# Kernel tuning notes

Measured on AMD Instinct MI355X. Metric: run time of the kernel, lower is better.

Reference implementation:

```python
import jax, jax.numpy as jnp
import numpy as np

D_MODEL = 1024
N_HEADS = 16
HEAD_DIM = D_MODEL // N_HEADS
B, L, E = 2, 2048, 256


def _linear_params(key, d_out, d_in):
    kw, kb = jax.random.split(key)
    lim = 1.0 / np.sqrt(d_in)
    W = jax.random.uniform(kw, (d_out, d_in), jnp.float32, -lim, lim)
    b = jax.random.uniform(kb, (d_out,), jnp.float32, -lim, lim)
    return W, b


def setup_inputs() -> dict:
    key = jax.random.key(0)
    ks = jax.random.split(key, 10)
    x = jax.random.normal(ks[0], (B, L, D_MODEL), jnp.float32)
    kg_embeds = jax.random.normal(ks[1], (B, E, D_MODEL), jnp.float32)
    Wq, bq = _linear_params(ks[2], D_MODEL, D_MODEL)
    Wk, bk = _linear_params(ks[3], D_MODEL, D_MODEL)
    Wv, bv = _linear_params(ks[4], D_MODEL, D_MODEL)
    Wo, bo = _linear_params(ks[5], D_MODEL, D_MODEL)
    Wkk, bkk = _linear_params(ks[6], D_MODEL, D_MODEL)
    Wkv, bkv = _linear_params(ks[7], D_MODEL, D_MODEL)
    Wg, bg = _linear_params(ks[8], D_MODEL, 2 * D_MODEL)
    return {"x": x, "kg_embeds": kg_embeds,
            "Wq": Wq, "bq": bq, "Wk": Wk, "bk": bk, "Wv": Wv, "bv": bv,
            "Wkk": Wkk, "bkk": bkk, "Wkv": Wkv, "bkv": bkv,
            "Wo": Wo, "bo": bo, "Wg": Wg, "bg": bg}


def _heads(t):
    # [B, S, D] -> [B, H, S, hd]
    Bb, S, _ = t.shape
    return t.reshape(Bb, S, N_HEADS, HEAD_DIM).transpose(0, 2, 1, 3)


def reference(x, kg_embeds, Wq, bq, Wk, bk, Wv, bv, Wkk, bkk, Wkv, bkv, Wo, bo, Wg, bg):
    scale = HEAD_DIM ** -0.5
    q = _heads(x @ Wq.T + bq)                      # [B,H,L,hd]
    k = _heads(x @ Wk.T + bk)
    v = _heads(x @ Wv.T + bv)
    k_kg = _heads(kg_embeds @ Wkk.T + bkk)         # [B,H,E,hd]
    v_kg = _heads(kg_embeds @ Wkv.T + bkv)
    k_aug = jnp.concatenate([k, k_kg], axis=2)     # [B,H,L+E,hd]
    v_aug = jnp.concatenate([v, v_kg], axis=2)
    scores = jnp.einsum('bhld,bhmd->bhlm', q, k_aug) * scale  # [B,H,L,L+E]
    attn = jax.nn.softmax(scores, axis=-1)
    out = jnp.einsum('bhlm,bhmd->bhld', attn, v_aug)           # [B,H,L,hd]
    out = out.transpose(0, 2, 1, 3).reshape(x.shape)            # [B,L,D]
    kg_global = jnp.broadcast_to(kg_embeds.mean(axis=1, keepdims=True), x.shape)
    gate = jax.nn.sigmoid(jnp.concatenate([out, kg_global], axis=-1) @ Wg.T + bg)
    return gate * (out @ Wo.T + bo) + (1.0 - gate) * x
```

## Files before the change

### kernel.cpp

```cpp
#include <hip/hip_runtime.h>
#include <stdint.h>

typedef unsigned short ushort_t;
typedef __attribute__((ext_vector_type(8))) short short8;
typedef __attribute__((ext_vector_type(4))) short short4v;
typedef __attribute__((ext_vector_type(4))) float f32x4;
typedef __attribute__((ext_vector_type(4))) unsigned uintx4;

#define DEV static __device__ __forceinline__

DEV unsigned short f2bf(float f) {
  unsigned u = __builtin_bit_cast(unsigned, f);
  u += 0x7fffu + ((u >> 16) & 1u);
  return (unsigned short)(u >> 16);
}
DEV float bf2f(unsigned short b) {
  return __builtin_bit_cast(float, (unsigned)b << 16);
}

DEV void gl16(const void* g, void* l) {
  __builtin_amdgcn_global_load_lds(
      (__attribute__((address_space(1))) char*)(unsigned long long)g,
      (__attribute__((address_space(3))) char*)(unsigned)(unsigned long long)l,
      16, 0, 0);
}

DEV f32x4 mfma_bf16(short8 a, short8 b, f32x4 c) {
  return __builtin_amdgcn_mfma_f32_16x16x32_bf16(a, b, c, 0, 0, 0);
}

DEV unsigned cvtpk(float lo, float hi) {
  unsigned r;
  asm("v_cvt_pk_bf16_f32 %0, %1, %2" : "=v"(r) : "v"(lo), "v"(hi));
  return r;
}
DEV void swap_net(unsigned& a, unsigned& b) {
  asm("v_permlane32_swap_b32 %0, %1" : "+v"(a), "+v"(b));
  asm("v_permlane16_swap_b32 %0, %1" : "+v"(a), "+v"(b));
}
DEV float redmax4(float x) {
  unsigned a = __builtin_bit_cast(unsigned, x), b = a;
  asm("v_permlane16_swap_b32 %0, %1" : "+v"(a), "+v"(b));
  float y = fmaxf(__builtin_bit_cast(float, a), __builtin_bit_cast(float, b));
  unsigned c = __builtin_bit_cast(unsigned, y), d = c;
  asm("v_permlane32_swap_b32 %0, %1" : "+v"(c), "+v"(d));
  return fmaxf(__builtin_bit_cast(float, c), __builtin_bit_cast(float, d));
}
DEV float lanebcast(float v, int srclane) {
  return __builtin_bit_cast(float,
      __builtin_amdgcn_ds_bpermute(srclane * 4, __builtin_bit_cast(int, v)));
}

__global__ __launch_bounds__(256) void k_cvt_all(
    const float* __restrict__ x, const float* __restrict__ kg,
    const float* __restrict__ Wq, const float* __restrict__ Wk, const float* __restrict__ Wv,
    const float* __restrict__ Wkk, const float* __restrict__ Wkv,
    const float* __restrict__ Wo, const float* __restrict__ Wg,
    ushort_t* __restrict__ xh, ushort_t* __restrict__ kgh,
    ushort_t* __restrict__ WB1, ushort_t* __restrict__ WB2, ushort_t* __restrict__ WB3) {
  const int b = blockIdx.x;
  if (b >= 10752) {
    const int i = (b - 10752) * 256 + threadIdx.x;
    const int r = i >> 8, c = (i & 255) * 4;
    const float4 v = *(const float4*)(Wg + (size_t)r * 2048 + c);
    short4v o;
    o.x = (short)f2bf(v.x); o.y = (short)f2bf(v.y); o.z = (short)f2bf(v.z); o.w = (short)f2bf(v.w);
    *(short4v*)(WB3 + 1048576 + (size_t)r * 1024 + c) = o;
    return;
  }
  const float* src;
  ushort_t* dst;
  int off;
  if (b < 4096)       { src = x;   dst = xh;            off = b; }
  else if (b < 4608)  { src = kg;  dst = kgh;           off = b - 4096; }
  else if (b < 5632)  { src = Wq;  dst = WB1;           off = b - 4608; }
  else if (b < 6656)  { src = Wk;  dst = WB1 + 1048576; off = b - 5632; }
  else if (b < 7680)  { src = Wv;  dst = WB1 + 2097152; off = b - 6656; }
  else if (b < 8704)  { src = Wkk; dst = WB2;           off = b - 7680; }
  else if (b < 9728)  { src = Wkv; dst = WB2 + 1048576; off = b - 8704; }
  else                { src = Wo;  dst = WB3;           off = b - 9728; }
  const int i = off * 1024 + threadIdx.x * 4;
  const float4 v = *(const float4*)(src + i);
  short4v o;
  o.x = (short)f2bf(v.x); o.y = (short)f2bf(v.y); o.z = (short)f2bf(v.z); o.w = (short)f2bf(v.w);
  *(short4v*)(dst + i) = o;
}

__global__ __launch_bounds__(256) void k_kgmean(const float* __restrict__ kg, float* __restrict__ out) {
  const int i = blockIdx.x * 256 + threadIdx.x;
  const int b = i >> 10, d = i & 1023;
  float s = 0.f;
  #pragma unroll 4
  for (int e = 0; e < 256; e++) s += kg[((size_t)b * 256 + e) * 1024 + d];
  out[i] = s * (1.0f / 256.0f);
}

__global__ __launch_bounds__(256) void k_g2(const float* __restrict__ kgm, const float* __restrict__ Wg,
                                            const float* __restrict__ bg, float* __restrict__ g2) {
  const int w = threadIdx.x >> 6, l = threadIdx.x & 63;
  const int idx = blockIdx.x * 4 + w;
  const int b = idx >> 10, n = idx & 1023;
  const float* wr = Wg + (size_t)n * 2048 + 1024;
  const float* mb = kgm + b * 1024;
  float s = 0.f;
  #pragma unroll
  for (int j = 0; j < 16; j++) s += mb[j * 64 + l] * wr[j * 64 + l];
  #pragma unroll
  for (int m = 32; m >= 1; m >>= 1) s += __shfl_xor(s, m);
  if (l == 0) g2[idx] = s + bg[n];
}

__global__ __launch_bounds__(256) void k_gemm_qkv(
    const ushort_t* __restrict__ xh, const ushort_t* __restrict__ WB1,
    const ushort_t* __restrict__ kgh, const ushort_t* __restrict__ WB2,
    const float* __restrict__ bq, const float* __restrict__ bk, const float* __restrict__ bv,
    const float* __restrict__ bkk, const float* __restrict__ bkv,
    ushort_t* __restrict__ Qg, ushort_t* __restrict__ Kaug, ushort_t* __restrict__ Vt) {
  const bool iskg = blockIdx.x >= 32;
  if (iskg && blockIdx.y >= 16) return;
  __shared__ __align__(16) ushort_t SH[16384];
  const int tid = threadIdx.x;
  const int w = tid >> 6, l = tid & 63;
  const int wr = w >> 1, wc = w & 1;
  const int fr = l & 15, fg = l >> 4;
  const int m0 = (iskg ? (blockIdx.x - 32) : blockIdx.x) * 128;
  const int n0 = blockIdx.y * 128;
  const int srow = tid >> 2, sseg = tid & 3;
  const ushort_t* A  = iskg ? kgh : xh;
  const ushort_t* Bw = iskg ? WB2 : WB1;
  const ushort_t* ga = A + (size_t)(m0 + srow) * 1024 + sseg * 8;
  const ushort_t* gb = Bw + (size_t)(n0 + srow) * 1024 + sseg * 8;
  f32x4 acc[4][4] = {};

  auto stage = [&](int nb, int kt) {
    char* lA = (char*)SH + nb * 8192 + w * 1024;
    char* lB = (char*)SH + 16384 + nb * 8192 + w * 1024;
    const ushort_t* gA = ga + kt * 32;
    const ushort_t* gB = gb + kt * 32;
    gl16(gA, lA);
    gl16(gA + 64 * 1024, lA + 4096);
    gl16(gB, lB);
    gl16(gB + 64 * 1024, lB + 4096);
  };

  stage(0, 0);
  __syncthreads();
  int cur = 0;
  for (int kt = 0; kt < 32; kt++) {
    if (kt < 31) stage(cur ^ 1, kt + 1);
    const short* Ab = (const short*)(SH + cur * 4096);
    const short* Bb = (const short*)(SH + 8192 + cur * 4096);
    short8 af[4], bfr[4];
    #pragma unroll
    for (int i = 0; i < 4; i++) {
      af[i]  = *(const short8*)(Ab + (wr * 64 + i * 16 + fr) * 32 + fg * 8);
      bfr[i] = *(const short8*)(Bb + (wc * 64 + i * 16 + fr) * 32 + fg * 8);
    }
    #pragma unroll
    for (int i = 0; i < 4; i++)
      #pragma unroll
      for (int j = 0; j < 4; j++)
        acc[i][j] = mfma_bf16(af[i], bfr[j], acc[i][j]);
    __syncthreads();
    cur ^= 1;
  }

  const int sec = n0 >> 10;
  const bool isV = iskg ? (sec == 1) : (sec == 2);

  if (isV) {
    const float* bV = iskg ? bkv : bv;
    #pragma unroll
    for (int i = 0; i < 4; i++) {
      #pragma unroll
      for (int j = 0; j < 4; j++) {
        const int ml0 = wr * 64 + i * 16 + fg * 4;
        const int nl = wc * 64 + j * 16 + fr;
        const float bb = bV[(n0 & 1023) + nl];
        short4v pk;
        #pragma unroll
        for (int r = 0; r < 4; r++) pk[r] = (short)f2bf(acc[i][j][r] + bb);
        *(short4v*)(SH + nl * 128 + (ml0 ^ ((nl & 7) << 3))) = pk;
      }
    }
    __syncthreads();
    const int row = tid >> 1, half = tid & 1;
    const int h = ((n0 & 1023) >> 6) + (row >> 6);
    const int d = row & 63;
    const int b = iskg ? (m0 >> 8) : (m0 >> 11);
    const int colbase = iskg ? (2048 + (m0 & 255)) : (m0 & 2047);
    ushort_t* dst = Vt + ((size_t)(b * 16 + h) * 64 + d) * 2304 + colbase + half * 64;
    const ushort_t* srow2 = SH + row * 128;
    #pragma unroll
    for (int k2 = 0; k2 < 8; k2++) {
      const int me = (half * 64 + k2 * 8) ^ ((row & 7) << 3);
      *(short8*)(dst + k2 * 8) = *(const short8*)(srow2 + me);
    }
    return;
  }

  #pragma unroll
  for (int i = 0; i < 4; i++) {
    #pragma unroll
    for (int j = 0; j < 4; j++) {
      #pragma unroll
      for (int r = 0; r < 4; r++) {
        const int m = m0 + wr * 64 + i * 16 + fg * 4 + r;
        const int nn = (n0 & 1023) + wc * 64 + j * 16 + fr;
        const int h = nn >> 6, d = nn & 63;
        const float v = acc[i][j][r];
        if (iskg) {
          const int b = m >> 8, e = m & 255;
          Kaug[((size_t)(b * 16 + h) * 2304 + 2048 + e) * 64 + d] = f2bf(v + bkk[nn]);
        } else {
          const int b = m >> 11, lq = m & 2047;
          if (sec == 0)
            Qg[((size_t)(b * 16 + h) * 2048 + lq) * 64 + d] = f2bf((v + bq[nn]) * 0.18033688f);
          else
            Kaug[((size_t)(b * 16 + h) * 2304 + lq) * 64 + d] = f2bf(v + bk[nn]);
        }
      }
    }
  }
}

__global__ __launch_bounds__(256) void k_gemm2(
    const ushort_t* __restrict__ A, const ushort_t* __restrict__ Bw,
    const float* __restrict__ bias0, const float* __restrict__ g2v,
    ushort_t* __restrict__ o0, ushort_t* __restrict__ o1) {
  __shared__ __align__(16) ushort_t As[2][128 * 32];
  __shared__ __align__(16) ushort_t Bs[2][128 * 32];
  const int tid = threadIdx.x;
  const int w = tid >> 6, l = tid & 63;
  const int wr = w >> 1, wc = w & 1;
  const int fr = l & 15, fg = l >> 4;
  const int m0 = blockIdx.x * 128, n0 = blockIdx.y * 128;
  const int srow = tid >> 2, sseg = tid & 3;
  const ushort_t* ga = A + (size_t)(m0 + srow) * 1024 + sseg * 8;
  const ushort_t* gb = Bw + (size_t)(n0 + srow) * 1024 + sseg * 8;
  f32x4 acc[4][4] = {};

  auto stage = [&](int nb, int kt) {
    char* lA = (char*)&As[nb][0] + w * 1024;
    char* lB = (char*)&Bs[nb][0] + w * 1024;
    const ushort_t* gA = ga + kt * 32;
    const ushort_t* gB = gb + kt * 32;
    gl16(gA, lA);
    gl16(gA + 64 * 1024, lA + 4096);
    gl16(gB, lB);
    gl16(gB + 64 * 1024, lB + 4096);
  };

  stage(0, 0);
  __syncthreads();
  int cur = 0;
  for (int kt = 0; kt < 32; kt++) {
    if (kt < 31) stage(cur ^ 1, kt + 1);
    const short* Ab = (const short*)&As[cur][0];
    const short* Bb = (const short*)&Bs[cur][0];
    short8 af[4], bfr[4];
    #pragma unroll
    for (int i = 0; i < 4; i++) {
      af[i]  = *(const short8*)(Ab + (wr * 64 + i * 16 + fr) * 32 + fg * 8);
      bfr[i] = *(const short8*)(Bb + (wc * 64 + i * 16 + fr) * 32 + fg * 8);
    }
    #pragma unroll
    for (int i = 0; i < 4; i++)
      #pragma unroll
      for (int j = 0; j < 4; j++)
        acc[i][j] = mfma_bf16(af[i], bfr[j], acc[i][j]);
    __syncthreads();
    cur ^= 1;
  }

  const int sec = n0 >> 10;
  #pragma unroll
  for (int i = 0; i < 4; i++) {
    #pragma unroll
    for (int j = 0; j < 4; j++) {
      #pragma unroll
      for (int r = 0; r < 4; r++) {
        const int m = m0 + wr * 64 + i * 16 + fg * 4 + r;
        const int nn = (n0 & 1023) + wc * 64 + j * 16 + fr;
        const float v = acc[i][j][r];
        if (sec == 0)
          o0[(size_t)m * 1024 + nn] = f2bf(v + bias0[nn]);
        else
          o1[(size_t)m * 1024 + nn] = f2bf(v + g2v[(m >> 11) * 1024 + nn]);
      }
    }
  }
}

__global__ __launch_bounds__(256, 4) void k_attn(
    const ushort_t* __restrict__ Qg, const ushort_t* __restrict__ Kg,
    const ushort_t* __restrict__ Vtg, ushort_t* __restrict__ Og) {
  __shared__ __align__(16) ushort_t Ks[2][64 * 64];
  __shared__ __align__(16) ushort_t Vs[2][64 * 64];
  const int tid = threadIdx.x;
  const int w = tid >> 6, l = tid & 63;
  const int fr = l & 15, fg = l >> 4;

  const int id = blockIdx.y * gridDim.x + blockIdx.x;
  const int bh = (id & 7) * 4 + ((id >> 3) >> 5);
  const int q0 = ((id >> 3) & 31) * 64 + w * 16;

  short8 qf[2];
  {
    const short* qrow = (const short*)(Qg + ((size_t)bh * 2048 + q0 + fr) * 64);
    qf[0] = *(const short8*)(qrow + fg * 8);
    qf[1] = *(const short8*)(qrow + 32 + fg * 8);
  }

  constexpr short ONE = 0x3F80;
  const short8 ones = {ONE, ONE, ONE, ONE, ONE, ONE, ONE, ONE};

  f32x4 o[4] = {};
  f32x4 lacc = {};
  float mrun = -1.0e30f;

  const int rsub = tid >> 3;
  const int cS = ((tid & 7) * 16) ^ ((rsub & 7) << 4);
  const char* kbase = (const char*)(Kg + (size_t)bh * 2304 * 64);
  const char* vbase = (const char*)(Vtg + (size_t)bh * 64 * 2304);

  auto stage = [&](int nb, int tile) {
    #pragma unroll
    for (int j = 0; j < 2; j++) {
      const int row = j * 32 + rsub;
      gl16(kbase + (size_t)(tile * 64 + row) * 128 + cS,
           (char*)&Ks[nb][0] + j * 4096 + tid * 16);
      gl16(vbase + (size_t)row * 4608 + tile * 128 + cS,
           (char*)&Vs[nb][0] + j * 4096 + tid * 16);
    }
  };

  stage(0, 0);

  const int rswz = (fr & 7) << 4;

  for (int mt = 0; mt < 36; mt++) {
    __syncthreads();
    if (mt < 35) stage((mt + 1) & 1, mt + 1);

    const char* Kb = (const char*)&Ks[mt & 1][0];
    const char* Vb = (const char*)&Vs[mt & 1][0];

    f32x4 s[4];
    #pragma unroll
    for (int t = 0; t < 4; t++) {
      const int rb = (t * 16 + fr) * 128 + fg * 16;
      const short8 k0 = *(const short8*)(Kb + (rb ^ rswz));
      const short8 k1 = *(const short8*)(Kb + ((rb + 64) ^ rswz));
      f32x4 z = {};
      z = mfma_bf16(k0, qf[0], z);
      z = mfma_bf16(k1, qf[1], z);
      s[t] = z;
    }

    float m = s[0][0];
    #pragma unroll
    for (int t = 0; t < 4; t++)
      #pragma unroll
      for (int r = 0; r < 4; r++) m = fmaxf(m, s[t][r]);
    const float mx = redmax4(m);
    if (__any(mx - mrun > 11.5416f)) {
      const float mn = fmaxf(mrun, mx);
      const float al = __builtin_amdgcn_exp2f(mrun - mn);
      mrun = mn;
      float ab[4];
      #pragma unroll
      for (int r = 0; r < 4; r++) ab[r] = lanebcast(al, fg * 4 + r);
      #pragma unroll
      for (int r = 0; r < 4; r++) {
        lacc[r] *= ab[r];
        #pragma unroll
        for (int dt = 0; dt < 4; dt++) o[dt][r] *= ab[r];
      }
    }
    #pragma unroll
    for (int t = 0; t < 4; t++)
      #pragma unroll
      for (int r = 0; r < 4; r++)
        s[t][r] = __builtin_amdgcn_exp2f(s[t][r] - mrun);

    #pragma unroll
    for (int c = 0; c < 2; c++) {
      unsigned a0 = cvtpk(s[2 * c][0], s[2 * c][1]);
      unsigned b0 = cvtpk(s[2 * c + 1][0], s[2 * c + 1][1]);
      unsigned a1 = cvtpk(s[2 * c][2], s[2 * c][3]);
      unsigned b1 = cvtpk(s[2 * c + 1][2], s[2 * c + 1][3]);
      swap_net(a0, b0);
      swap_net(a1, b1);
      uintx4 u;
      u.x = a0; u.y = a1; u.z = b0; u.w = b1;
      const short8 pf = __builtin_bit_cast(short8, u);
      lacc = mfma_bf16(pf, ones, lacc);
      #pragma unroll
      for (int dt = 0; dt < 4; dt++) {
        const int vb2 = ((dt * 16 + fr) * 128) + fg * 16 + c * 64;
        const short8 vf = *(const short8*)(Vb + (vb2 ^ rswz));
        o[dt] = mfma_bf16(pf, vf, o[dt]);
      }
    }
  }

  const int b = bh >> 4, h = bh & 15;
  #pragma unroll
  for (int r = 0; r < 4; r++) {
    const float inv = 1.0f / lacc[r];
    const int q = q0 + fg * 4 + r;
    ushort_t* orow = Og + ((size_t)b * 2048 + q) * 1024 + h * 64;
    #pragma unroll
    for (int dt = 0; dt < 4; dt++) orow[dt * 16 + fr] = f2bf(o[dt][r] * inv);
  }
}

__global__ __launch_bounds__(256) void k_final(const float* __restrict__ x,
                                               const ushort_t* __restrict__ OUT,
                                               const ushort_t* __restrict__ GL,
                                               float* __restrict__ y) {
  const int i = (blockIdx.x * 256 + threadIdx.x) * 4;
  const float4 xv = *(const float4*)(x + i);
  const short4v ov = *(const short4v*)((const short*)OUT + i);
  const short4v gv = *(const short4v*)((const short*)GL + i);
  float4 r;
  {
    const float o0 = bf2f((unsigned short)ov.x);
    const float g0 = 1.f / (1.f + __expf(-bf2f((unsigned short)gv.x)));
    r.x = xv.x + g0 * (o0 - xv.x);
  }
  {
    const float o1 = bf2f((unsigned short)ov.y);
    const float g1 = 1.f / (1.f + __expf(-bf2f((unsigned short)gv.y)));
    r.y = xv.y + g1 * (o1 - xv.y);
  }
  {
    const float o2 = bf2f((unsigned short)ov.z);
    const float g2 = 1.f / (1.f + __expf(-bf2f((unsigned short)gv.z)));
    r.z = xv.z + g2 * (o2 - xv.z);
  }
  {
    const float o3 = bf2f((unsigned short)ov.w);
    const float g3 = 1.f / (1.f + __expf(-bf2f((unsigned short)gv.w)));
    r.w = xv.w + g3 * (o3 - xv.w);
  }
  *(float4*)(y + i) = r;
}

extern "C" void kernel_launch(void* const* d_in, const int* in_sizes, int n_in,
                              void* d_out, int out_size, void* d_ws, size_t ws_size,
                              hipStream_t stream) {
  (void)in_sizes; (void)n_in; (void)out_size; (void)ws_size;
  const float* x   = (const float*)d_in[0];
  const float* kg  = (const float*)d_in[1];
  const float* Wq  = (const float*)d_in[2];
  const float* bq  = (const float*)d_in[3];
  const float* Wk  = (const float*)d_in[4];
  const float* bk  = (const float*)d_in[5];
  const float* Wv  = (const float*)d_in[6];
  const float* bv  = (const float*)d_in[7];
  const float* Wkk = (const float*)d_in[8];
  const float* bkk = (const float*)d_in[9];
  const float* Wkv = (const float*)d_in[10];
  const float* bkv = (const float*)d_in[11];
  const float* Wo  = (const float*)d_in[12];
  const float* bo  = (const float*)d_in[13];
  const float* Wg  = (const float*)d_in[14];
  const float* bg  = (const float*)d_in[15];
  float* y = (float*)d_out;

  char* ws = (char*)d_ws;
  size_t off = 0;
  auto take = [&](size_t bytes) {
    char* p = ws + off;
    off += (bytes + 255) & ~(size_t)255;
    return p;
  };
  ushort_t* xh   = (ushort_t*)take((size_t)4096 * 1024 * 2);
  ushort_t* kgh  = (ushort_t*)take((size_t)512 * 1024 * 2);
  ushort_t* WB1  = (ushort_t*)take((size_t)3072 * 1024 * 2);
  ushort_t* WB2  = (ushort_t*)take((size_t)2048 * 1024 * 2);
  ushort_t* WB3  = (ushort_t*)take((size_t)2048 * 1024 * 2);
  ushort_t* Qg   = (ushort_t*)take((size_t)32 * 2048 * 64 * 2);
  ushort_t* Kaug = (ushort_t*)take((size_t)32 * 2304 * 64 * 2);
  ushort_t* Vt   = (ushort_t*)take((size_t)32 * 2304 * 64 * 2);
  ushort_t* Og   = (ushort_t*)take((size_t)4096 * 1024 * 2);
  ushort_t* OUTb = (ushort_t*)take((size_t)4096 * 1024 * 2);
  ushort_t* GLb  = (ushort_t*)take((size_t)4096 * 1024 * 2);
  float* kgm     = (float*)take(2048 * 4);
  float* g2      = (float*)take(2048 * 4);

  k_cvt_all<<<11776, 256, 0, stream>>>(x, kg, Wq, Wk, Wv, Wkk, Wkv, Wo, Wg,
                                       xh, kgh, WB1, WB2, WB3);
  k_kgmean<<<8, 256, 0, stream>>>(kg, kgm);
  k_g2<<<512, 256, 0, stream>>>(kgm, Wg, bg, g2);

  k_gemm_qkv<<<dim3(36, 24), 256, 0, stream>>>(xh, WB1, kgh, WB2,
                                               bq, bk, bv, bkk, bkv, Qg, Kaug, Vt);
  k_attn<<<dim3(32, 32), 256, 0, stream>>>(Qg, Kaug, Vt, Og);
  k_gemm2<<<dim3(32, 16), 256, 0, stream>>>(Og, WB3, bo, g2, OUTb, GLb);
  k_final<<<4096, 256, 0, stream>>>(x, OUTb, GLb, y);
}
```

Measured before the change: 190.6 us.

## Replace both projection GEMMs with 256x256-tile, triple-buffered templated kernel

Replaces the QKV and output/gate GEMM kernels with one templated kernel. It uses 256x256 tiles, 512 threads, a three-stage global_load_lds pipeline with explicit vmcnt waits, an XOR-swizzled LDS layout, and a block-index remap that spreads tiles across XCDs. Larger tiles raise arithmetic intensity and cut global reloads of A and B. The cost is only 208 and 128 blocks launched, fewer than the CU count, and 128KB of LDS per block, which caps occupancy at one block per CU.

```diff
diff --git a/kernel.cpp b/kernel.cpp
--- a/kernel.cpp
+++ b/kernel.cpp
@@ -110,183 +110,162 @@
   if (l == 0) g2[idx] = s + bg[n];
 }
 
-__global__ __launch_bounds__(256) void k_gemm_qkv(
-    const ushort_t* __restrict__ xh, const ushort_t* __restrict__ WB1,
-    const ushort_t* __restrict__ kgh, const ushort_t* __restrict__ WB2,
-    const float* __restrict__ bq, const float* __restrict__ bk, const float* __restrict__ bv,
-    const float* __restrict__ bkk, const float* __restrict__ bkv,
-    ushort_t* __restrict__ Qg, ushort_t* __restrict__ Kaug, ushort_t* __restrict__ Vt) {
-  const bool iskg = blockIdx.x >= 32;
-  if (iskg && blockIdx.y >= 16) return;
-  __shared__ __align__(16) ushort_t SH[16384];
+template <int MODE>
+__global__ __launch_bounds__(512, 2) void k_mm256(
+    const ushort_t* __restrict__ A0, const ushort_t* __restrict__ B0,
+    const ushort_t* __restrict__ A1, const ushort_t* __restrict__ B1,
+    const float* __restrict__ f0, const float* __restrict__ f1, const float* __restrict__ f2,
+    const float* __restrict__ f3, const float* __restrict__ f4,
+    ushort_t* __restrict__ o0, ushort_t* __restrict__ o1, ushort_t* __restrict__ o2) {
+  __shared__ __align__(16) char SHb[131072];
   const int tid = threadIdx.x;
   const int w = tid >> 6, l = tid & 63;
-  const int wr = w >> 1, wc = w & 1;
+  const int wr = w >> 2, wc = w & 3;
   const int fr = l & 15, fg = l >> 4;
-  const int m0 = (iskg ? (blockIdx.x - 32) : blockIdx.x) * 128;
-  const int n0 = blockIdx.y * 128;
-  const int srow = tid >> 2, sseg = tid & 3;
-  const ushort_t* A  = iskg ? kgh : xh;
-  const ushort_t* Bw = iskg ? WB2 : WB1;
-  const ushort_t* ga = A + (size_t)(m0 + srow) * 1024 + sseg * 8;
-  const ushort_t* gb = Bw + (size_t)(n0 + srow) * 1024 + sseg * 8;
-  f32x4 acc[4][4] = {};
-
-  auto stage = [&](int nb, int kt) {
-    char* lA = (char*)SH + nb * 8192 + w * 1024;
-    char* lB = (char*)SH + 16384 + nb * 8192 + w * 1024;
-    const ushort_t* gA = ga + kt * 32;
-    const ushort_t* gB = gb + kt * 32;
-    gl16(gA, lA);
-    gl16(gA + 64 * 1024, lA + 4096);
-    gl16(gB, lB);
-    gl16(gB + 64 * 1024, lB + 4096);
+
+  int m0, n0row, iskg = 0, by;
+  if (MODE == 0) {
+    const int wg = ((int)blockIdx.x & 7) * 26 + ((int)blockIdx.x >> 3);
+    if (wg < 192) { const int bx = wg / 12; by = wg % 12; m0 = bx * 256; }
+    else          { const int k = wg - 192; iskg = 1; by = k & 7; m0 = (k >> 3) * 256; }
+    n0row = by * 256;
+  } else {
+    const int wg = ((int)blockIdx.x & 7) * 16 + ((int)blockIdx.x >> 3);
+    by = wg & 7; m0 = (wg >> 3) * 256; n0row = by * 256;
+  }
+  const ushort_t* A = (MODE == 0 && iskg) ? A1 : A0;
+  const ushort_t* B = (MODE == 0 && iskg) ? B1 : B0;
+
+  int grow[2], gcb[2];
+  #pragma unroll
+  for (int j = 0; j < 2; j++) {
+    const int beta = j * 512 + tid;
+    const int rp = beta >> 3;
+    const int u = (beta & 7) ^ (rp & 7);
+    grow[j] = 2 * rp + (u >> 2);
+    gcb[j] = u & 3;
+  }
+  const char* gA[2];
+  const char* gB[2];
+  #pragma unroll
+  for (int j = 0; j < 2; j++) {
+    gA[j] = (const char*)A + (size_t)(m0 + grow[j]) * 2048 + gcb[j] * 16;
+    gB[j] = (const char*)B + (size_t)(n0row + grow[j]) * 2048 + gcb[j] * 16;
+  }
+  const int dstoff0 = w * 1024 + l * 16;
+
+  auto stage = [&](int s, int kt) {
+    char* As = SHb + s * 32768;
+    char* Bs = As + 16384;
+    const int ko = kt * 64;
+    #pragma unroll
+    for (int j = 0; j < 2; j++) {
+      gl16(gA[j] + ko, As + j * 8192 + dstoff0);
+      gl16(gB[j] + ko, Bs + j * 8192 + dstoff0);
+    }
   };
 
+  int aoff[8], boff[4];
+  #pragma unroll
+  for (int i = 0; i < 8; i++) {
+    const int row = wr * 128 + i * 16 + fr;
+    aoff[i] = (row >> 1) * 128 + ((((row & 1) << 6) | (fg << 4)) ^ (((row >> 1) & 7) << 4));
+  }
+  #pragma unroll
+  for (int j = 0; j < 4; j++) {
+    const int row = wc * 64 + j * 16 + fr;
+    boff[j] = (row >> 1) * 128 + ((((row & 1) << 6) | (fg << 4)) ^ (((row >> 1) & 7) << 4));
+  }
+
+  f32x4 acc[8][4] = {};
+
   stage(0, 0);
+  stage(1, 1);
+  int sc = 0, sn2 = 2;
+  for (int kt = 0; kt < 32; kt++) {
+    if (kt < 31) asm volatile("s_waitcnt vmcnt(4)" ::: "memory");
+    else         asm volatile("s_waitcnt vmcnt(0)" ::: "memory");
+    __builtin_amdgcn_s_barrier();
+    asm volatile("" ::: "memory");
+    if (kt <= 29) stage(sn2, kt + 2);
+    const char* Ab = SHb + sc * 32768;
+    const char* Bb = Ab + 16384;
+    short8 af[8], bf[4];
+    #pragma unroll
+    for (int j = 0; j < 4; j++) bf[j] = *(const short8*)(Bb + boff[j]);
+    #pragma unroll
+    for (int i = 0; i < 8; i++) af[i] = *(const short8*)(Ab + aoff[i]);
+    #pragma unroll
+    for (int i = 0; i < 8; i++)
+      #pragma unroll
+      for (int j = 0; j < 4; j++)
+        acc[i][j] = mfma_bf16(af[i], bf[j], acc[i][j]);
+    sc++; if (sc == 3) sc = 0;
+    sn2++; if (sn2 == 3) sn2 = 0;
+  }
   __syncthreads();
-  int cur = 0;
-  for (int kt = 0; kt < 32; kt++) {
-    if (kt < 31) stage(cur ^ 1, kt + 1);
-    const short* Ab = (const short*)(SH + cur * 4096);
-    const short* Bb = (const short*)(SH + 8192 + cur * 4096);
-    short8 af[4], bfr[4];
-    #pragma unroll
-    for (int i = 0; i < 4; i++) {
-      af[i]  = *(const short8*)(Ab + (wr * 64 + i * 16 + fr) * 32 + fg * 8);
-      bfr[i] = *(const short8*)(Bb + (wc * 64 + i * 16 + fr) * 32 + fg * 8);
-    }
-    #pragma unroll
-    for (int i = 0; i < 4; i++)
-      #pragma unroll
-      for (int j = 0; j < 4; j++)
-        acc[i][j] = mfma_bf16(af[i], bfr[j], acc[i][j]);
-    __syncthreads();
-    cur ^= 1;
-  }
-
-  const int sec = n0 >> 10;
-  const bool isV = iskg ? (sec == 1) : (sec == 2);
+
+  const int sec = (MODE == 0) ? (iskg ? (by >> 2) + 10 : (by >> 2)) : (by >> 2);
+  const int nnbase = (by & 3) * 256;
+  const bool isV = (MODE == 0) && (sec == 2 || sec == 11);
 
   if (isV) {
-    const float* bV = iskg ? bkv : bv;
-    #pragma unroll
-    for (int i = 0; i < 4; i++) {
+    ushort_t* SHs = (ushort_t*)SHb;
+    const float* bV = iskg ? f4 : f2;
+    const int bidx = iskg ? (m0 >> 8) : (m0 >> 11);
+    const int colbase = iskg ? (2048 + (m0 & 255)) : (m0 & 2047);
+    #pragma unroll
+    for (int i = 0; i < 8; i++) {
       #pragma unroll
       for (int j = 0; j < 4; j++) {
-        const int ml0 = wr * 64 + i * 16 + fg * 4;
         const int nl = wc * 64 + j * 16 + fr;
-        const float bb = bV[(n0 & 1023) + nl];
+        const int ml0 = wr * 128 + i * 16 + fg * 4;
+        const float bb = bV[nnbase + nl];
         short4v pk;
         #pragma unroll
         for (int r = 0; r < 4; r++) pk[r] = (short)f2bf(acc[i][j][r] + bb);
-        *(short4v*)(SH + nl * 128 + (ml0 ^ ((nl & 7) << 3))) = pk;
+        *(short4v*)(SHs + nl * 256 + (ml0 ^ ((nl & 7) << 3))) = pk;
       }
     }
     __syncthreads();
-    const int row = tid >> 1, half = tid & 1;
-    const int h = ((n0 & 1023) >> 6) + (row >> 6);
-    const int d = row & 63;
-    const int b = iskg ? (m0 >> 8) : (m0 >> 11);
-    const int colbase = iskg ? (2048 + (m0 & 255)) : (m0 & 2047);
-    ushort_t* dst = Vt + ((size_t)(b * 16 + h) * 64 + d) * 2304 + colbase + half * 64;
-    const ushort_t* srow2 = SH + row * 128;
-    #pragma unroll
-    for (int k2 = 0; k2 < 8; k2++) {
-      const int me = (half * 64 + k2 * 8) ^ ((row & 7) << 3);
-      *(short8*)(dst + k2 * 8) = *(const short8*)(srow2 + me);
+    const int nl = tid >> 1, mh = tid & 1;
+    const int n = nnbase + nl;
+    const int h = n >> 6, d = n & 63;
+    ushort_t* dst = o2 + ((size_t)(bidx * 16 + h) * 64 + d) * 2304 + colbase + mh * 128;
+    const ushort_t* srcr = SHs + nl * 256;
+    #pragma unroll
+    for (int k2 = 0; k2 < 16; k2++) {
+      const int me = (mh * 128 + k2 * 8) ^ ((nl & 7) << 3);
+      *(short8*)(dst + k2 * 8) = *(const short8*)(srcr + me);
     }
     return;
   }
 
   #pragma unroll
-  for (int i = 0; i < 4; i++) {
+  for (int i = 0; i < 8; i++) {
     #pragma unroll
     for (int j = 0; j < 4; j++) {
+      const int nn = nnbase + wc * 64 + j * 16 + fr;
+      const int h = nn >> 6, d = nn & 63;
       #pragma unroll
       for (int r = 0; r < 4; r++) {
-        const int m = m0 + wr * 64 + i * 16 + fg * 4 + r;
-        const int nn = (n0 & 1023) + wc * 64 + j * 16 + fr;
-        const int h = nn >> 6, d = nn & 63;
+        const int m = m0 + wr * 128 + i * 16 + fg * 4 + r;
         const float v = acc[i][j][r];
-        if (iskg) {
-          const int b = m >> 8, e = m & 255;
-          Kaug[((size_t)(b * 16 + h) * 2304 + 2048 + e) * 64 + d] = f2bf(v + bkk[nn]);
+        if (MODE == 0) {
+          if (sec == 0) {
+            const int b = m >> 11, lq = m & 2047;
+            o0[((size_t)(b * 16 + h) * 2048 + lq) * 64 + d] = f2bf((v + f0[nn]) * 0.18033688f);
+          } else if (sec == 1) {
+            const int b = m >> 11, lq = m & 2047;
+            o1[((size_t)(b * 16 + h) * 2304 + lq) * 64 + d] = f2bf(v + f1[nn]);
+          } else {
+            const int b = m >> 8, e = m & 255;
+            o1[((size_t)(b * 16 + h) * 2304 + 2048 + e) * 64 + d] = f2bf(v + f3[nn]);
+          }
         } else {
-          const int b = m >> 11, lq = m & 2047;
-          if (sec == 0)
-            Qg[((size_t)(b * 16 + h) * 2048 + lq) * 64 + d] = f2bf((v + bq[nn]) * 0.18033688f);
-          else
-            Kaug[((size_t)(b * 16 + h) * 2304 + lq) * 64 + d] = f2bf(v + bk[nn]);
+          if (sec == 0) o0[(size_t)m * 1024 + nn] = f2bf(v + f0[nn]);
+          else          o1[(size_t)m * 1024 + nn] = f2bf(v + f1[(m >> 11) * 1024 + nn]);
         }
-      }
-    }
-  }
-}
-
-__global__ __launch_bounds__(256) void k_gemm2(
-    const ushort_t* __restrict__ A, const ushort_t* __restrict__ Bw,
-    const float* __restrict__ bias0, const float* __restrict__ g2v,
-    ushort_t* __restrict__ o0, ushort_t* __restrict__ o1) {
-  __shared__ __align__(16) ushort_t As[2][128 * 32];
-  __shared__ __align__(16) ushort_t Bs[2][128 * 32];
-  const int tid = threadIdx.x;
-  const int w = tid >> 6, l = tid & 63;
-  const int wr = w >> 1, wc = w & 1;
-  const int fr = l & 15, fg = l >> 4;
-  const int m0 = blockIdx.x * 128, n0 = blockIdx.y * 128;
-  const int srow = tid >> 2, sseg = tid & 3;
-  const ushort_t* ga = A + (size_t)(m0 + srow) * 1024 + sseg * 8;
-  const ushort_t* gb = Bw + (size_t)(n0 + srow) * 1024 + sseg * 8;
-  f32x4 acc[4][4] = {};
-
-  auto stage = [&](int nb, int kt) {
-    char* lA = (char*)&As[nb][0] + w * 1024;
-    char* lB = (char*)&Bs[nb][0] + w * 1024;
-    const ushort_t* gA = ga + kt * 32;
-    const ushort_t* gB = gb + kt * 32;
-    gl16(gA, lA);
-    gl16(gA + 64 * 1024, lA + 4096);
-    gl16(gB, lB);
-    gl16(gB + 64 * 1024, lB + 4096);
-  };
-
-  stage(0, 0);
-  __syncthreads();
-  int cur = 0;
-  for (int kt = 0; kt < 32; kt++) {
-    if (kt < 31) stage(cur ^ 1, kt + 1);
-    const short* Ab = (const short*)&As[cur][0];
-    const short* Bb = (const short*)&Bs[cur][0];
-    short8 af[4], bfr[4];
-    #pragma unroll
-    for (int i = 0; i < 4; i++) {
-      af[i]  = *(const short8*)(Ab + (wr * 64 + i * 16 + fr) * 32 + fg * 8);
-      bfr[i] = *(const short8*)(Bb + (wc * 64 + i * 16 + fr) * 32 + fg * 8);
-    }
-    #pragma unroll
-    for (int i = 0; i < 4; i++)
-      #pragma unroll
-      for (int j = 0; j < 4; j++)
-        acc[i][j] = mfma_bf16(af[i], bfr[j], acc[i][j]);
-    __syncthreads();
-    cur ^= 1;
-  }
-
-  const int sec = n0 >> 10;
-  #pragma unroll
-  for (int i = 0; i < 4; i++) {
-    #pragma unroll
-    for (int j = 0; j < 4; j++) {
-      #pragma unroll
-      for (int r = 0; r < 4; r++) {
-        const int m = m0 + wr * 64 + i * 16 + fg * 4 + r;
-        const int nn = (n0 & 1023) + wc * 64 + j * 16 + fr;
-        const float v = acc[i][j][r];
-        if (sec == 0)
-          o0[(size_t)m * 1024 + nn] = f2bf(v + bias0[nn]);
-        else
-          o1[(size_t)m * 1024 + nn] = f2bf(v + g2v[(m >> 11) * 1024 + nn]);
       }
     }
   }
@@ -496,9 +475,10 @@
   k_kgmean<<<8, 256, 0, stream>>>(kg, kgm);
   k_g2<<<512, 256, 0, stream>>>(kgm, Wg, bg, g2);
 
-  k_gemm_qkv<<<dim3(36, 24), 256, 0, stream>>>(xh, WB1, kgh, WB2,
-                                               bq, bk, bv, bkk, bkv, Qg, Kaug, Vt);
+  k_mm256<0><<<208, 512, 0, stream>>>(xh, WB1, kgh, WB2,
+                                      bq, bk, bv, bkk, bkv, Qg, Kaug, Vt);
   k_attn<<<dim3(32, 32), 256, 0, stream>>>(Qg, Kaug, Vt, Og);
-  k_gemm2<<<dim3(32, 16), 256, 0, stream>>>(Og, WB3, bo, g2, OUTb, GLb);
+  k_mm256<1><<<128, 512, 0, stream>>>(Og, WB3, nullptr, nullptr,
+                                      bo, g2, nullptr, nullptr, nullptr, OUTb, GLb, nullptr);
   k_final<<<4096, 256, 0, stream>>>(x, OUTb, GLb, y);
 }
```

Result: slower. 201.4 us (+5.7%).
